# Optimization experiments

Measured on AMD Instinct MI355X. Metric: run time of the kernel, lower is better.

The kernel has to match this reference:

```python
import jax, jax.numpy as jnp
import numpy as np

B, L, C = 4, 4096, 64

def setup_inputs() -> dict:
    key = jax.random.key(0)
    ks = jax.random.split(key, 7)
    s = 1.0 / np.sqrt(C)
    return {
        "x": jax.random.normal(ks[0], (B, L, C), dtype=jnp.float32),
        "Wq": jax.random.normal(ks[1], (C, C), dtype=jnp.float32) * s,
        "bq": jnp.zeros((C,), dtype=jnp.float32),
        "Wk": jax.random.normal(ks[2], (C, C), dtype=jnp.float32) * s,
        "bk": jnp.zeros((C,), dtype=jnp.float32),
        "Wv": jax.random.normal(ks[3], (C, C), dtype=jnp.float32) * s,
        "bv": jnp.zeros((C,), dtype=jnp.float32),
    }

def reference(x, Wq, bq, Wk, bk, Wv, bv):
    # Conv1D kernel_size=1 == pointwise linear over channels
    Q = jnp.einsum('blc,cf->blf', x, Wq) + bq  # [B, L, F]
    K = jnp.einsum('blc,cf->blf', x, Wk) + bk
    V = jnp.einsum('blc,cf->blf', x, Wv) + bv
    F = Wq.shape[1]
    scores = jnp.einsum('bqf,bkf->bqk', Q, K) / jnp.sqrt(jnp.float32(F))  # [B, Lq, Lk]
    # NOTE: original uses tf.keras.layers.Softmax(axis=1) -> normalize over QUERY axis
    attn = jax.nn.softmax(scores, axis=1)
    out = jnp.einsum('bqk,bkf->bqf', attn, V)
    return out + x
```

## Files before the change

### kernel.cpp

```cpp
#include <hip/hip_runtime.h>
#include <math.h>


#define BB 4
#define LL 4096
#define CC 64
#define C2 0.18033688011112042f

typedef __attribute__((ext_vector_type(8)))  short bf16x8;
typedef __attribute__((ext_vector_type(4)))  float f32x4;
typedef __attribute__((ext_vector_type(16))) float f32x16;
typedef __attribute__((ext_vector_type(4)))  unsigned int u32x4;

#define MFMA16(a, b, c) __builtin_amdgcn_mfma_f32_16x16x32_bf16(a, b, c, 0, 0, 0)
#define MFMA32(a, b, c) __builtin_amdgcn_mfma_f32_32x32x16_bf16(a, b, c, 0, 0, 0)
#define EXP2(x) __builtin_amdgcn_exp2f(x)

#define GLD4(dst, voff, base, imm) \
    asm volatile("global_load_dwordx4 %0, %1, %2 offset:%c3" \
                 : "=v"(dst) : "v"(voff), "s"(base), "i"(imm))
#define WAITVM0() asm volatile("s_waitcnt vmcnt(0)" ::: "memory")
#define SBAR() __builtin_amdgcn_sched_barrier(0)
#define PRIO(n) __builtin_amdgcn_s_setprio(n)

static __device__ __forceinline__ bf16x8 asbf(u32x4 v) {
    union { u32x4 a; bf16x8 b; } u; u.a = v; return u.b;
}
static __device__ __forceinline__ unsigned short f2bf(float f) {
    union { float f; unsigned u; } v; v.f = f;
    unsigned r = v.u + 0x7FFFu + ((v.u >> 16) & 1u);
    return (unsigned short)(r >> 16);
}
static __device__ __forceinline__ float bf2f(unsigned short h) {
    union { unsigned u; float f; } v; v.u = ((unsigned)h) << 16; return v.f;
}
static __device__ __forceinline__ bf16x8 pack8(float4 a, float4 b) {
    bf16x8 r;
    r[0] = (short)f2bf(a.x); r[1] = (short)f2bf(a.y);
    r[2] = (short)f2bf(a.z); r[3] = (short)f2bf(a.w);
    r[4] = (short)f2bf(b.x); r[5] = (short)f2bf(b.y);
    r[6] = (short)f2bf(b.z); r[7] = (short)f2bf(b.w);
    return r;
}
static __device__ __forceinline__ unsigned cvtpk(float lo, float hi) {
    unsigned r;
    asm("v_cvt_pk_bf16_f32 %0, %1, %2" : "=v"(r) : "v"(lo), "v"(hi));
    return r;
}
static __device__ __forceinline__ bf16x8 lds_frag(const unsigned short* p) {
    union { uint2 u[2]; bf16x8 b; } t;
    t.u[0] = *(const uint2*)(p);
    t.u[1] = *(const uint2*)(p + 4);
    return t.b;
}
static __device__ __forceinline__ void lds_put(unsigned short* p, u32x4 v) {
    *(uint2*)(p)     = make_uint2(v[0], v[1]);
    *(uint2*)(p + 4) = make_uint2(v[2], v[3]);
}

__global__ __launch_bounds__(512) void k_qkv(
    const float* __restrict__ x,
    const float* __restrict__ Wq, const float* __restrict__ bq,
    const float* __restrict__ Wk, const float* __restrict__ bk,
    const float* __restrict__ Wv, const float* __restrict__ bv,
    unsigned short* __restrict__ Qb, unsigned short* __restrict__ Kb,
    unsigned short* __restrict__ Vt)
{
    __shared__ float Wl[64 * 64];
    __shared__ unsigned short ldsV[64 * 72];
    const int bid = blockIdx.x;
    const int mat = bid % 3;
    const int r0 = (bid / 3) * 64;
    const int tid = threadIdx.x, w = tid >> 6, lane = tid & 63;
    const int c = lane & 15, g = lane >> 4;
    const int rw = (w >> 1) * 16;
    const int c0 = (w & 1) * 32;

    const float* W  = (mat == 0) ? Wq : (mat == 1) ? Wk : Wv;
    const float* bs = (mat == 0) ? bq : (mat == 1) ? bk : bv;

    {
        const float4* wsrc = (const float4*)W;
        float4* wdst = (float4*)Wl;
        wdst[tid] = wsrc[tid];
        wdst[tid + 512] = wsrc[tid + 512];
    }

    const float* xr = x + (size_t)(r0 + rw + c) * CC;
    const bf16x8 ax0 = pack8(((const float4*)xr)[2 * g], ((const float4*)xr)[2 * g + 1]);
    const bf16x8 ax1 = pack8(((const float4*)xr)[8 + 2 * g], ((const float4*)xr)[8 + 2 * g + 1]);
    __syncthreads();

    f32x4 acc0 = {0.f, 0.f, 0.f, 0.f}, acc1 = {0.f, 0.f, 0.f, 0.f};
    {
        const int col = c0 + c;
        bf16x8 b0, b1;
        #pragma unroll
        for (int j = 0; j < 8; ++j) {
            b0[j] = (short)f2bf(Wl[(8 * g + j) * 64 + col]);
            b1[j] = (short)f2bf(Wl[(32 + 8 * g + j) * 64 + col]);
        }
        acc0 = MFMA16(ax0, b0, acc0); acc0 = MFMA16(ax1, b1, acc0);
    }
    {
        const int col = c0 + 16 + c;
        bf16x8 b0, b1;
        #pragma unroll
        for (int j = 0; j < 8; ++j) {
            b0[j] = (short)f2bf(Wl[(8 * g + j) * 64 + col]);
            b1[j] = (short)f2bf(Wl[(32 + 8 * g + j) * 64 + col]);
        }
        acc1 = MFMA16(ax0, b0, acc1); acc1 = MFMA16(ax1, b1, acc1);
    }
    const float bias0 = bs[c0 + c], bias1 = bs[c0 + 16 + c];

    if (mat < 2) {
        unsigned short* dst = (mat == 0) ? Qb : Kb;
        #pragma unroll
        for (int r = 0; r < 4; ++r) {
            const size_t row = (size_t)(r0 + rw + 4 * g + r) * CC;
            dst[row + c0 + c]      = f2bf(acc0[r] + bias0);
            dst[row + c0 + 16 + c] = f2bf(acc1[r] + bias1);
        }
    } else {
        #pragma unroll
        for (int r = 0; r < 4; ++r) {
            const int rowin = rw + 4 * g + r;
            ldsV[(c0 + c) * 72 + rowin]      = f2bf(acc0[r] + bias0);
            ldsV[(c0 + 16 + c) * 72 + rowin] = f2bf(acc1[r] + bias1);
        }
        __syncthreads();
        const int b = r0 >> 12, ktb = (r0 & 4095) >> 5;
        const int h = tid >> 8, f = (tid >> 2) & 63, ch = tid & 3;
        *(uint4*)(Vt + ((size_t)(b * 128 + ktb + h) * 64 + f) * 32 + ch * 8)
            = *(const uint4*)(ldsV + f * 72 + h * 32 + ch * 8);
    }
}

__global__ __launch_bounds__(512, 4) void k_stats(
    const unsigned short* __restrict__ Qb, const unsigned short* __restrict__ Kb,
    unsigned short* __restrict__ Vt)
{
    const int nb = ((blockIdx.x & 7) << 6) | (blockIdx.x >> 3);
    const int b = nb >> 7, kt32 = nb & 127;
    const int kbase = kt32 * 32;
    const int tid = threadIdx.x, w = tid >> 6, lane = tid & 63;
    const int l31 = lane & 31, hi = lane >> 5;

    __shared__ unsigned short qsm[8][2][32 * 68];
    __shared__ float pl[8][32];
    __shared__ float rls[32];

    const unsigned short* kr = Kb + ((size_t)b * LL + kbase + l31) * CC + 8 * hi;
    const bf16x8 ak0 = *(const bf16x8*)(kr);
    const bf16x8 ak1 = *(const bf16x8*)(kr + 16);
    const bf16x8 ak2 = *(const bf16x8*)(kr + 32);
    const bf16x8 ak3 = *(const bf16x8*)(kr + 48);

    const unsigned short* const sQ = Qb + (size_t)b * LL * CC;
    const unsigned wqoff = (unsigned)(w * 65536);
    const int wb = (lane >> 3) * 68 + (lane & 7) * 8;
    unsigned short* const q0b = &qsm[w][0][0];
    unsigned short* const q1b = &qsm[w][1][0];

    u32x4 S0, S1, S2, S3;
    #define QISS(s_) do { \
        const unsigned vo = wqoff + (unsigned)((s_) * 4096 + lane * 16); \
        GLD4(S0, vo, sQ, 0);    GLD4(S1, vo, sQ, 1024); \
        GLD4(S2, vo, sQ, 2048); GLD4(S3, vo, sQ, 3072); \
    } while (0)
    #define QWR(dst) do { \
        unsigned short* _p = (dst) + wb; \
        lds_put(_p, S0);        lds_put(_p + 544, S1); \
        lds_put(_p + 1088, S2); lds_put(_p + 1632, S3); \
    } while (0)

    QISS(0); WAITVM0(); SBAR(); QWR(q0b); QISS(1);

    f32x16 lacc = {};
    for (int s = 0; s < 16; ++s) {
        const unsigned short* qp = ((s & 1) ? q1b : q0b) + l31 * 68 + hi * 8;
        const bf16x8 b0 = lds_frag(qp);
        const bf16x8 b1 = lds_frag(qp + 16);
        const bf16x8 b2 = lds_frag(qp + 32);
        const bf16x8 b3 = lds_frag(qp + 48);
        f32x16 T = {};
        PRIO(1);
        T = MFMA32(ak0, b0, T); T = MFMA32(ak1, b1, T);
        T = MFMA32(ak2, b2, T); T = MFMA32(ak3, b3, T);
        PRIO(0);
        #pragma unroll
        for (int r = 0; r < 16; ++r) lacc[r] += EXP2(T[r] * C2);
        if (s < 15) {
            WAITVM0(); SBAR();
            QWR((s & 1) ? q0b : q1b);
            if (s < 14) QISS(s + 2);
        }
    }
    #undef QISS
    #undef QWR

    #pragma unroll
    for (int r = 0; r < 16; ++r) {
        float v = lacc[r];
        v += __shfl_xor(v, 1);  v += __shfl_xor(v, 2);
        v += __shfl_xor(v, 4);  v += __shfl_xor(v, 8);
        v += __shfl_xor(v, 16);
        lacc[r] = v;
    }
    if (l31 == 0) {
        #pragma unroll
        for (int r = 0; r < 16; ++r)
            pl[w][(r & 3) + 8 * (r >> 2) + 4 * hi] = lacc[r];
    }
    __syncthreads();
    if (tid < 32) {
        float L = 0.f;
        #pragma unroll
        for (int ww = 0; ww < 8; ++ww) L += pl[ww][tid];
        rls[tid] = 1.0f / L;
    }
    __syncthreads();

    {
        unsigned short* vbase = Vt + ((size_t)(b * 128 + kt32)) * 2048;
        const int kin0 = (tid & 7) * 4;
        ushort4 v = *(const ushort4*)(vbase + tid * 4);
        v.x = f2bf(bf2f(v.x) * rls[kin0 + 0]);
        v.y = f2bf(bf2f(v.y) * rls[kin0 + 1]);
        v.z = f2bf(bf2f(v.z) * rls[kin0 + 2]);
        v.w = f2bf(bf2f(v.w) * rls[kin0 + 3]);
        *(ushort4*)(vbase + tid * 4) = v;
    }
}

__global__ __launch_bounds__(512, 2) void k_out(
    const float* __restrict__ x,
    const unsigned short* __restrict__ Qb, const unsigned short* __restrict__ Kb,
    const unsigned short* __restrict__ Vt,
    float* __restrict__ out)
{
    const int nb = ((blockIdx.x & 7) << 6) | (blockIdx.x >> 3);
    const int b = nb >> 7, qt = nb & 127;
    const int q0 = qt * 32;
    const int tid = threadIdx.x, w = tid >> 6, lane = tid & 63;
    const int l31 = lane & 31, hi = lane >> 5;

    __shared__ unsigned short ksm[8][2][32 * 68];
    __shared__ unsigned short vsm[8][2][64 * 36];

    const unsigned short* qr = Qb + ((size_t)b * LL + q0 + l31) * CC + 8 * hi;
    const bf16x8 qb0 = *(const bf16x8*)(qr);
    const bf16x8 qb1 = *(const bf16x8*)(qr + 16);
    const bf16x8 qb2 = *(const bf16x8*)(qr + 32);
    const bf16x8 qb3 = *(const bf16x8*)(qr + 48);

    const unsigned short* const sK = Kb + (size_t)b * LL * CC;
    const unsigned short* const sV = Vt + (size_t)b * 128 * 2048;
    const unsigned wkoff = (unsigned)(w * 65536);
    const unsigned wvoff = (unsigned)(w * 65536);
    const int kwb = (lane >> 3) * 68 + (lane & 7) * 8;
    const int vwb = (lane >> 2) * 36 + (lane & 3) * 8;

    u32x4 K0, K1, K2, K3, V0, V1, V2, V3;
    #define KISS(s_) do { \
        const unsigned vo = wkoff + (unsigned)((s_) * 4096 + lane * 16); \
        GLD4(K0, vo, sK, 0);    GLD4(K1, vo, sK, 1024); \
        GLD4(K2, vo, sK, 2048); GLD4(K3, vo, sK, 3072); \
    } while (0)
    #define VISS(s_) do { \
        const unsigned vo = wvoff + (unsigned)((s_) * 4096 + lane * 16); \
        GLD4(V0, vo, sV, 0);    GLD4(V1, vo, sV, 1024); \
        GLD4(V2, vo, sV, 2048); GLD4(V3, vo, sV, 3072); \
    } while (0)
    #define KWR(dst) do { \
        unsigned short* _p = (dst) + kwb; \
        lds_put(_p, K0);        lds_put(_p + 544, K1); \
        lds_put(_p + 1088, K2); lds_put(_p + 1632, K3); \
    } while (0)
    #define VWR(dst) do { \
        unsigned short* _p = (dst) + vwb; \
        lds_put(_p, V0);        lds_put(_p + 576, V1); \
        lds_put(_p + 1152, V2); lds_put(_p + 1728, V3); \
    } while (0)

    KISS(0); VISS(0); WAITVM0(); SBAR();
    KWR(&ksm[w][0][0]); VWR(&vsm[w][0][0]);
    KISS(1); VISS(1);

    f32x16 oacc0 = {}, oacc1 = {};

    for (int s = 0; s < 16; ++s) {
        const unsigned short* Kt = &ksm[w][s & 1][0];
        const unsigned short* Vl = &vsm[w][s & 1][0];
        const unsigned short* kp = Kt + l31 * 68 + hi * 8;
        const bf16x8 a0 = lds_frag(kp);
        const bf16x8 a1 = lds_frag(kp + 16);
        const bf16x8 a2 = lds_frag(kp + 32);
        const bf16x8 a3 = lds_frag(kp + 48);
        f32x16 T = {};
        PRIO(1);
        T = MFMA32(a0, qb0, T); T = MFMA32(a1, qb1, T);
        T = MFMA32(a2, qb2, T); T = MFMA32(a3, qb3, T);
        PRIO(0);
        unsigned u0 = cvtpk(EXP2(T[0] * C2),  EXP2(T[1] * C2));
        unsigned u1 = cvtpk(EXP2(T[2] * C2),  EXP2(T[3] * C2));
        unsigned u2 = cvtpk(EXP2(T[4] * C2),  EXP2(T[5] * C2));
        unsigned u3 = cvtpk(EXP2(T[6] * C2),  EXP2(T[7] * C2));
        unsigned u4 = cvtpk(EXP2(T[8] * C2),  EXP2(T[9] * C2));
        unsigned u5 = cvtpk(EXP2(T[10] * C2), EXP2(T[11] * C2));
        unsigned u6 = cvtpk(EXP2(T[12] * C2), EXP2(T[13] * C2));
        unsigned u7 = cvtpk(EXP2(T[14] * C2), EXP2(T[15] * C2));
        asm volatile("s_nop 1");
        asm("v_permlane32_swap_b32 %0, %1" : "+v"(u0), "+v"(u2));
        asm("v_permlane32_swap_b32 %0, %1" : "+v"(u1), "+v"(u3));
        asm("v_permlane32_swap_b32 %0, %1" : "+v"(u4), "+v"(u6));
        asm("v_permlane32_swap_b32 %0, %1" : "+v"(u5), "+v"(u7));
        u32x4 f1, f2;
        f1[0] = u0; f1[1] = u1; f1[2] = u2; f1[3] = u3;
        f2[0] = u4; f2[1] = u5; f2[2] = u6; f2[3] = u7;
        const unsigned short* vp0 = Vl + l31 * 36 + hi * 8;
        const unsigned short* vp1 = Vl + (32 + l31) * 36 + hi * 8;
        const bf16x8 v00 = lds_frag(vp0);
        const bf16x8 v01 = lds_frag(vp0 + 16);
        const bf16x8 v10 = lds_frag(vp1);
        const bf16x8 v11 = lds_frag(vp1 + 16);
        PRIO(1);
        oacc0 = MFMA32(v00, asbf(f1), oacc0);
        oacc0 = MFMA32(v01, asbf(f2), oacc0);
        oacc1 = MFMA32(v10, asbf(f1), oacc1);
        oacc1 = MFMA32(v11, asbf(f2), oacc1);
        PRIO(0);
        if (s < 15) {
            WAITVM0(); SBAR();
            KWR(&ksm[w][(s + 1) & 1][0]);
            VWR(&vsm[w][(s + 1) & 1][0]);
            if (s < 14) { KISS(s + 2); VISS(s + 2); }
        }
    }
    #undef KISS
    #undef VISS
    #undef KWR
    #undef VWR

    __syncthreads();
    float* ocomb = (float*)&ksm[0][0][0];
    for (int i = tid; i < 32 * 68; i += 512) ocomb[i] = 0.f;
    __syncthreads();
    #pragma unroll
    for (int r = 0; r < 16; ++r) {
        const int fr = (r & 3) + 8 * (r >> 2) + 4 * hi;
        atomicAdd(&ocomb[l31 * 68 + fr],      oacc0[r]);
        atomicAdd(&ocomb[l31 * 68 + 32 + fr], oacc1[r]);
    }
    __syncthreads();
    {
        const int q = tid >> 4, fc = tid & 15;
        const size_t row = (size_t)b * LL + q0 + q;
        const float4 xv = ((const float4*)(x + row * CC))[fc];
        const float4 ov = *(const float4*)(&ocomb[q * 68 + fc * 4]);
        ((float4*)(out + row * CC))[fc] =
            make_float4(xv.x + ov.x, xv.y + ov.y, xv.z + ov.z, xv.w + ov.w);
    }
}

extern "C" void kernel_launch(void* const* d_in, const int* in_sizes, int n_in,
                              void* d_out, int out_size, void* d_ws, size_t ws_size,
                              hipStream_t stream)
{
    const float* x  = (const float*)d_in[0];
    const float* Wq = (const float*)d_in[1];
    const float* bq = (const float*)d_in[2];
    const float* Wk = (const float*)d_in[3];
    const float* bk = (const float*)d_in[4];
    const float* Wv = (const float*)d_in[5];
    const float* bv = (const float*)d_in[6];
    float* out = (float*)d_out;

    const size_t n = (size_t)BB * LL * CC;
    unsigned short* Qb = (unsigned short*)d_ws;
    unsigned short* Kb = Qb + n;
    unsigned short* Vt = Kb + n;

    hipLaunchKernelGGL(k_qkv, dim3(3 * BB * LL / 64), dim3(512), 0, stream,
                       x, Wq, bq, Wk, bk, Wv, bv, Qb, Kb, Vt);
    hipLaunchKernelGGL(k_stats, dim3(BB * (LL / 32)), dim3(512), 0, stream,
                       Qb, Kb, Vt);
    hipLaunchKernelGGL(k_out, dim3(BB * (LL / 32)), dim3(512), 0, stream,
                       x, Qb, Kb, Vt, out);
}
```

Baseline: 104.4 us.

## Process 64 queries per block in k_out to reuse K/V tiles

Each k_out block now handles two 32-query sub-tiles (A and B) sharing the same K and V tiles loaded from global memory into LDS. This halves the grid and halves the K/V traffic per query. The LDS staging drops from double to single buffering, which is safe because each wave rewrites only its own region after its reads have been consumed. The cost is more registers per thread, only 256 blocks, and less latency hiding from the removed double buffer.

```diff
diff --git a/kernel.cpp b/kernel.cpp
--- a/kernel.cpp
+++ b/kernel.cpp
@@ -240,20 +240,25 @@
     const unsigned short* __restrict__ Vt,
     float* __restrict__ out)
 {
-    const int nb = ((blockIdx.x & 7) << 6) | (blockIdx.x >> 3);
-    const int b = nb >> 7, qt = nb & 127;
-    const int q0 = qt * 32;
+    const int nb = ((blockIdx.x & 7) << 5) | (blockIdx.x >> 3);
+    const int b = nb >> 6, qt = nb & 63;
+    const int q0 = qt * 64;
     const int tid = threadIdx.x, w = tid >> 6, lane = tid & 63;
     const int l31 = lane & 31, hi = lane >> 5;
 
-    __shared__ unsigned short ksm[8][2][32 * 68];
-    __shared__ unsigned short vsm[8][2][64 * 36];
-
-    const unsigned short* qr = Qb + ((size_t)b * LL + q0 + l31) * CC + 8 * hi;
-    const bf16x8 qb0 = *(const bf16x8*)(qr);
-    const bf16x8 qb1 = *(const bf16x8*)(qr + 16);
-    const bf16x8 qb2 = *(const bf16x8*)(qr + 32);
-    const bf16x8 qb3 = *(const bf16x8*)(qr + 48);
+    __shared__ unsigned short ksm[8][32 * 68];
+    __shared__ unsigned short vsm[8][64 * 36];
+
+    const unsigned short* qrA = Qb + ((size_t)b * LL + q0 + l31) * CC + 8 * hi;
+    const unsigned short* qrB = qrA + 32 * CC;
+    const bf16x8 qA0 = *(const bf16x8*)(qrA);
+    const bf16x8 qA1 = *(const bf16x8*)(qrA + 16);
+    const bf16x8 qA2 = *(const bf16x8*)(qrA + 32);
+    const bf16x8 qA3 = *(const bf16x8*)(qrA + 48);
+    const bf16x8 qB0 = *(const bf16x8*)(qrB);
+    const bf16x8 qB1 = *(const bf16x8*)(qrB + 16);
+    const bf16x8 qB2 = *(const bf16x8*)(qrB + 32);
+    const bf16x8 qB3 = *(const bf16x8*)(qrB + 48);
 
     const unsigned short* const sK = Kb + (size_t)b * LL * CC;
     const unsigned short* const sV = Vt + (size_t)b * 128 * 2048;
@@ -273,68 +278,85 @@
         GLD4(V0, vo, sV, 0);    GLD4(V1, vo, sV, 1024); \
         GLD4(V2, vo, sV, 2048); GLD4(V3, vo, sV, 3072); \
     } while (0)
-    #define KWR(dst) do { \
-        unsigned short* _p = (dst) + kwb; \
+    #define KWR() do { \
+        unsigned short* _p = &ksm[w][0] + kwb; \
         lds_put(_p, K0);        lds_put(_p + 544, K1); \
         lds_put(_p + 1088, K2); lds_put(_p + 1632, K3); \
     } while (0)
-    #define VWR(dst) do { \
-        unsigned short* _p = (dst) + vwb; \
+    #define VWR() do { \
+        unsigned short* _p = &vsm[w][0] + vwb; \
         lds_put(_p, V0);        lds_put(_p + 576, V1); \
         lds_put(_p + 1152, V2); lds_put(_p + 1728, V3); \
     } while (0)
 
     KISS(0); VISS(0); WAITVM0(); SBAR();
-    KWR(&ksm[w][0][0]); VWR(&vsm[w][0][0]);
+    KWR(); VWR();
     KISS(1); VISS(1);
 
-    f32x16 oacc0 = {}, oacc1 = {};
+    f32x16 oA0 = {}, oA1 = {}, oB0 = {}, oB1 = {};
 
     for (int s = 0; s < 16; ++s) {
-        const unsigned short* Kt = &ksm[w][s & 1][0];
-        const unsigned short* Vl = &vsm[w][s & 1][0];
-        const unsigned short* kp = Kt + l31 * 68 + hi * 8;
+        const unsigned short* kp = &ksm[w][0] + l31 * 68 + hi * 8;
         const bf16x8 a0 = lds_frag(kp);
         const bf16x8 a1 = lds_frag(kp + 16);
         const bf16x8 a2 = lds_frag(kp + 32);
         const bf16x8 a3 = lds_frag(kp + 48);
-        f32x16 T = {};
+        f32x16 TA = {}, TB = {};
         PRIO(1);
-        T = MFMA32(a0, qb0, T); T = MFMA32(a1, qb1, T);
-        T = MFMA32(a2, qb2, T); T = MFMA32(a3, qb3, T);
+        TA = MFMA32(a0, qA0, TA); TA = MFMA32(a1, qA1, TA);
+        TA = MFMA32(a2, qA2, TA); TA = MFMA32(a3, qA3, TA);
+        TB = MFMA32(a0, qB0, TB); TB = MFMA32(a1, qB1, TB);
+        TB = MFMA32(a2, qB2, TB); TB = MFMA32(a3, qB3, TB);
         PRIO(0);
-        unsigned u0 = cvtpk(EXP2(T[0] * C2),  EXP2(T[1] * C2));
-        unsigned u1 = cvtpk(EXP2(T[2] * C2),  EXP2(T[3] * C2));
-        unsigned u2 = cvtpk(EXP2(T[4] * C2),  EXP2(T[5] * C2));
-        unsigned u3 = cvtpk(EXP2(T[6] * C2),  EXP2(T[7] * C2));
-        unsigned u4 = cvtpk(EXP2(T[8] * C2),  EXP2(T[9] * C2));
-        unsigned u5 = cvtpk(EXP2(T[10] * C2), EXP2(T[11] * C2));
-        unsigned u6 = cvtpk(EXP2(T[12] * C2), EXP2(T[13] * C2));
-        unsigned u7 = cvtpk(EXP2(T[14] * C2), EXP2(T[15] * C2));
+        unsigned a0u = cvtpk(EXP2(TA[0] * C2),  EXP2(TA[1] * C2));
+        unsigned a1u = cvtpk(EXP2(TA[2] * C2),  EXP2(TA[3] * C2));
+        unsigned a2u = cvtpk(EXP2(TA[4] * C2),  EXP2(TA[5] * C2));
+        unsigned a3u = cvtpk(EXP2(TA[6] * C2),  EXP2(TA[7] * C2));
+        unsigned a4u = cvtpk(EXP2(TA[8] * C2),  EXP2(TA[9] * C2));
+        unsigned a5u = cvtpk(EXP2(TA[10] * C2), EXP2(TA[11] * C2));
+        unsigned a6u = cvtpk(EXP2(TA[12] * C2), EXP2(TA[13] * C2));
+        unsigned a7u = cvtpk(EXP2(TA[14] * C2), EXP2(TA[15] * C2));
+        unsigned b0u = cvtpk(EXP2(TB[0] * C2),  EXP2(TB[1] * C2));
+        unsigned b1u = cvtpk(EXP2(TB[2] * C2),  EXP2(TB[3] * C2));
+        unsigned b2u = cvtpk(EXP2(TB[4] * C2),  EXP2(TB[5] * C2));
+        unsigned b3u = cvtpk(EXP2(TB[6] * C2),  EXP2(TB[7] * C2));
+        unsigned b4u = cvtpk(EXP2(TB[8] * C2),  EXP2(TB[9] * C2));
+        unsigned b5u = cvtpk(EXP2(TB[10] * C2), EXP2(TB[11] * C2));
+        unsigned b6u = cvtpk(EXP2(TB[12] * C2), EXP2(TB[13] * C2));
+        unsigned b7u = cvtpk(EXP2(TB[14] * C2), EXP2(TB[15] * C2));
         asm volatile("s_nop 1");
-        asm("v_permlane32_swap_b32 %0, %1" : "+v"(u0), "+v"(u2));
-        asm("v_permlane32_swap_b32 %0, %1" : "+v"(u1), "+v"(u3));
-        asm("v_permlane32_swap_b32 %0, %1" : "+v"(u4), "+v"(u6));
-        asm("v_permlane32_swap_b32 %0, %1" : "+v"(u5), "+v"(u7));
-        u32x4 f1, f2;
-        f1[0] = u0; f1[1] = u1; f1[2] = u2; f1[3] = u3;
-        f2[0] = u4; f2[1] = u5; f2[2] = u6; f2[3] = u7;
-        const unsigned short* vp0 = Vl + l31 * 36 + hi * 8;
-        const unsigned short* vp1 = Vl + (32 + l31) * 36 + hi * 8;
+        asm("v_permlane32_swap_b32 %0, %1" : "+v"(a0u), "+v"(a2u));
+        asm("v_permlane32_swap_b32 %0, %1" : "+v"(a1u), "+v"(a3u));
+        asm("v_permlane32_swap_b32 %0, %1" : "+v"(a4u), "+v"(a6u));
+        asm("v_permlane32_swap_b32 %0, %1" : "+v"(a5u), "+v"(a7u));
+        asm("v_permlane32_swap_b32 %0, %1" : "+v"(b0u), "+v"(b2u));
+        asm("v_permlane32_swap_b32 %0, %1" : "+v"(b1u), "+v"(b3u));
+        asm("v_permlane32_swap_b32 %0, %1" : "+v"(b4u), "+v"(b6u));
+        asm("v_permlane32_swap_b32 %0, %1" : "+v"(b5u), "+v"(b7u));
+        u32x4 fA1, fA2, fB1, fB2;
+        fA1[0] = a0u; fA1[1] = a1u; fA1[2] = a2u; fA1[3] = a3u;
+        fA2[0] = a4u; fA2[1] = a5u; fA2[2] = a6u; fA2[3] = a7u;
+        fB1[0] = b0u; fB1[1] = b1u; fB1[2] = b2u; fB1[3] = b3u;
+        fB2[0] = b4u; fB2[1] = b5u; fB2[2] = b6u; fB2[3] = b7u;
+        const unsigned short* vp0 = &vsm[w][0] + l31 * 36 + hi * 8;
+        const unsigned short* vp1 = &vsm[w][0] + (32 + l31) * 36 + hi * 8;
         const bf16x8 v00 = lds_frag(vp0);
         const bf16x8 v01 = lds_frag(vp0 + 16);
         const bf16x8 v10 = lds_frag(vp1);
         const bf16x8 v11 = lds_frag(vp1 + 16);
         PRIO(1);
-        oacc0 = MFMA32(v00, asbf(f1), oacc0);
-        oacc0 = MFMA32(v01, asbf(f2), oacc0);
-        oacc1 = MFMA32(v10, asbf(f1), oacc1);
-        oacc1 = MFMA32(v11, asbf(f2), oacc1);
+        oA0 = MFMA32(v00, asbf(fA1), oA0);
+        oA0 = MFMA32(v01, asbf(fA2), oA0);
+        oA1 = MFMA32(v10, asbf(fA1), oA1);
+        oA1 = MFMA32(v11, asbf(fA2), oA1);
+        oB0 = MFMA32(v00, asbf(fB1), oB0);
+        oB0 = MFMA32(v01, asbf(fB2), oB0);
+        oB1 = MFMA32(v10, asbf(fB1), oB1);
+        oB1 = MFMA32(v11, asbf(fB2), oB1);
         PRIO(0);
         if (s < 15) {
             WAITVM0(); SBAR();
-            KWR(&ksm[w][(s + 1) & 1][0]);
-            VWR(&vsm[w][(s + 1) & 1][0]);
+            KWR(); VWR();
             if (s < 14) { KISS(s + 2); VISS(s + 2); }
         }
     }
@@ -344,23 +366,29 @@
     #undef VWR
 
     __syncthreads();
-    float* ocomb = (float*)&ksm[0][0][0];
-    for (int i = tid; i < 32 * 68; i += 512) ocomb[i] = 0.f;
+    float* ocomb = (float*)&ksm[0][0];
+    for (int i = tid; i < 64 * 68; i += 512) ocomb[i] = 0.f;
     __syncthreads();
     #pragma unroll
     for (int r = 0; r < 16; ++r) {
         const int fr = (r & 3) + 8 * (r >> 2) + 4 * hi;
-        atomicAdd(&ocomb[l31 * 68 + fr],      oacc0[r]);
-        atomicAdd(&ocomb[l31 * 68 + 32 + fr], oacc1[r]);
+        atomicAdd(&ocomb[l31 * 68 + fr],             oA0[r]);
+        atomicAdd(&ocomb[l31 * 68 + 32 + fr],        oA1[r]);
+        atomicAdd(&ocomb[(32 + l31) * 68 + fr],      oB0[r]);
+        atomicAdd(&ocomb[(32 + l31) * 68 + 32 + fr], oB1[r]);
     }
     __syncthreads();
     {
-        const int q = tid >> 4, fc = tid & 15;
+        const int q = tid >> 3, f8 = (tid & 7) * 8;
         const size_t row = (size_t)b * LL + q0 + q;
-        const float4 xv = ((const float4*)(x + row * CC))[fc];
-        const float4 ov = *(const float4*)(&ocomb[q * 68 + fc * 4]);
-        ((float4*)(out + row * CC))[fc] =
-            make_float4(xv.x + ov.x, xv.y + ov.y, xv.z + ov.z, xv.w + ov.w);
+        const float4 xv0 = ((const float4*)(x + row * CC))[f8 >> 2];
+        const float4 xv1 = ((const float4*)(x + row * CC))[(f8 >> 2) + 1];
+        const float4 ov0 = *(const float4*)(&ocomb[q * 68 + f8]);
+        const float4 ov1 = *(const float4*)(&ocomb[q * 68 + f8 + 4]);
+        ((float4*)(out + row * CC))[f8 >> 2] =
+            make_float4(xv0.x + ov0.x, xv0.y + ov0.y, xv0.z + ov0.z, xv0.w + ov0.w);
+        ((float4*)(out + row * CC))[(f8 >> 2) + 1] =
+            make_float4(xv1.x + ov1.x, xv1.y + ov1.y, xv1.z + ov1.z, xv1.w + ov1.w);
     }
 }
 
@@ -386,6 +414,6 @@
                        x, Wq, bq, Wk, bk, Wv, bv, Qb, Kb, Vt);
     hipLaunchKernelGGL(k_stats, dim3(BB * (LL / 32)), dim3(512), 0, stream,
                        Qb, Kb, Vt);
-    hipLaunchKernelGGL(k_out, dim3(BB * (LL / 32)), dim3(512), 0, stream,
+    hipLaunchKernelGGL(k_out, dim3(BB * (LL / 64)), dim3(512), 0, stream,
                        x, Qb, Kb, Vt, out);
 }
```

Measured after the change: 97.07 us. -7.0%, faster.
